# Performance work log

Hardware: AMD Instinct MI355X
Metric: run time of the kernel (lower is better)

The kernel has to match this reference:

```python
import jax, jax.numpy as jnp
import numpy as np

NUM_HEADS = 4  # init kwarg num_heads


def setup_inputs() -> dict:
    key = jax.random.key(0)
    ks = jax.random.split(key, 9)
    B, N, C, S1 = 8, 2048, 128, 3  # S1 = scale + 1
    w = 1.0 / np.sqrt(C)
    return {
        "pcd": jax.random.normal(ks[0], (B, N, C), jnp.float32),
        "coordinate": jax.random.normal(ks[1], (B, N, 3), jnp.float32),
        "K": 16,
        "Wq": jax.random.normal(ks[2], (C, C), jnp.float32) * w,
        "bq": jax.random.normal(ks[3], (C,), jnp.float32) * w,
        "Wk": jax.random.normal(ks[4], (S1, C, C), jnp.float32) * w,
        "bk": jax.random.normal(ks[5], (S1, C), jnp.float32) * w,
        "Wv": jax.random.normal(ks[6], (C, C), jnp.float32) * w,
        "bv": jax.random.normal(ks[7], (C,), jnp.float32) * w,
    }


def reference(pcd, coordinate, K, Wq, bq, Wk, bk, Wv, bv):
    B, N, C = pcd.shape
    S1 = Wk.shape[0]            # scale + 1
    H = NUM_HEADS
    D = C // H                  # head_dim
    Kt = K * S1                 # one KNN shared by all scales ('OneK')

    # --- KNN in coordinate space (squared euclidean) ---
    sq = jnp.sum(coordinate * coordinate, axis=-1)                      # [B,N]
    dist = sq[:, :, None] + sq[:, None, :] \
        - 2.0 * jnp.einsum('bnc,bmc->bnm', coordinate, coordinate)      # [B,N,N]
    _, idx = jax.lax.top_k(-dist, Kt)                                   # [B,N,Kt]

    # --- gather neighbor features, group_type='diff' (neighbor - center) ---
    nb = jax.vmap(lambda f, i: f[i])(pcd, idx)                          # [B,N,Kt,C]
    diff = nb - pcd[:, :, None, :]                                      # [B,N,Kt,C]

    q = (pcd @ Wq + bq).reshape(B, N, H, D)                             # [B,N,H,D]
    v = (pcd @ Wv + bv).reshape(B, N, H, D)                             # [B,N,H,D]
    inv_sqrt_d = 1.0 / jnp.sqrt(jnp.asarray(D, pcd.dtype))

    # --- per-scale attention maps ('multiple' mode), summed to a per-head gate ---
    attn_map = jnp.zeros((B, N, H), pcd.dtype)
    for i in range(S1):
        feats = diff[:, :, i * K:(i + 1) * K, :]                        # [B,N,K,C]
        k_i = (feats @ Wk[i] + bk[i]).reshape(B, N, K, H, D)            # [B,N,K,H,D]
        logits = jnp.einsum('bnhd,bnkhd->bnhk', q, k_i) * inv_sqrt_d    # [B,N,H,K]
        a = jax.nn.softmax(logits, axis=-1)
        attn_map = attn_map + jnp.sum(a * logits, axis=-1)              # [B,N,H]

    # matmul(attn[...,1,1], value[...,1,D]) -> per-head scalar gate on value
    out = attn_map[..., None] * v                                       # [B,N,H,D]
    return out.reshape(B, N, H * D)
```

## Files before the change

### kernel.cpp

```cpp
#include <hip/hip_runtime.h>
#include <hip/hip_bf16.h>
#include <cstdint>
#include <cstddef>

#define NB_B 8
#define NB_N 2048
#define NB_C 128
#define NB_H 4
#define NB_D 32
#define NB_S1 3
#define NB_K 16
#define NB_KT 48
#define INV_SQRT_D 0.17677669529663688f

#define DPP_F(x, ctrl) \
  __int_as_float(__builtin_amdgcn_update_dpp(0, __float_as_int(x), ctrl, 0xF, 0xF, true))

__device__ __forceinline__ float sum16(float x) {
  x += DPP_F(x, 0xB1);
  x += DPP_F(x, 0x4E);
  x += DPP_F(x, 0x141);
  x += DPP_F(x, 0x140);
  return x;
}
__device__ __forceinline__ float max16(float x) {
  x = fmaxf(x, DPP_F(x, 0xB1));
  x = fmaxf(x, DPP_F(x, 0x4E));
  x = fmaxf(x, DPP_F(x, 0x141));
  x = fmaxf(x, DPP_F(x, 0x140));
  return x;
}

__device__ __forceinline__ unsigned long long u64min(unsigned long long a,
                                                     unsigned long long b) {
  return a < b ? a : b;
}
__device__ __forceinline__ unsigned long long u64max(unsigned long long a,
                                                     unsigned long long b) {
  return a > b ? a : b;
}

__device__ __forceinline__ unsigned int dpp32(unsigned int x, int sel) {
  if (sel == 0)
    return (unsigned int)__builtin_amdgcn_update_dpp(0, (int)x, 0xB1, 0xF, 0xF, true);
  return (unsigned int)__builtin_amdgcn_update_dpp(0, (int)x, 0x4E, 0xF, 0xF, true);
}
__device__ __forceinline__ unsigned long long lane_xor64(unsigned long long v, int lx) {
  if (lx == 32) return __shfl_xor(v, 32);
  unsigned int lo = (unsigned int)v, hi = (unsigned int)(v >> 32);
  switch (lx) {
    case 1:  lo = dpp32(lo, 0); hi = dpp32(hi, 0); break;
    case 2:  lo = dpp32(lo, 1); hi = dpp32(hi, 1); break;
    case 4:
      lo = (unsigned int)__builtin_amdgcn_ds_swizzle((int)lo, 0x101F);
      hi = (unsigned int)__builtin_amdgcn_ds_swizzle((int)hi, 0x101F);
      break;
    case 8:
      lo = (unsigned int)__builtin_amdgcn_ds_swizzle((int)lo, 0x201F);
      hi = (unsigned int)__builtin_amdgcn_ds_swizzle((int)hi, 0x201F);
      break;
    default:
      lo = (unsigned int)__builtin_amdgcn_ds_swizzle((int)lo, 0x401F);
      hi = (unsigned int)__builtin_amdgcn_ds_swizzle((int)hi, 0x401F);
      break;
  }
  return ((unsigned long long)hi << 32) | lo;
}

__device__ __forceinline__ void bitonic128(unsigned long long& v0,
                                           unsigned long long& v1, int L) {
#pragma unroll
  for (int k = 2; k <= 128; k <<= 1) {
#pragma unroll
    for (int j = k >> 1; j > 0; j >>= 1) {
      bool up = ((L & (k >> 1)) == 0);
      if (j == 1) {
        unsigned long long lo = u64min(v0, v1), hi = u64max(v0, v1);
        v0 = up ? lo : hi;
        v1 = up ? hi : lo;
      } else {
        int lx = j >> 1;
        unsigned long long o0 = lane_xor64(v0, lx);
        unsigned long long o1 = lane_xor64(v1, lx);
        bool keepmin = (((L & lx) == 0) == up);
        v0 = keepmin ? u64min(v0, o0) : u64max(v0, o0);
        v1 = keepmin ? u64min(v1, o1) : u64max(v1, o1);
      }
    }
  }
}

__global__ __launch_bounds__(256) void prep_kernel(const float* __restrict__ coord,
                                                   const float* __restrict__ Wk,
                                                   float* __restrict__ sq,
                                                   float* __restrict__ wkT) {
  int tid = blockIdx.x * 256 + threadIdx.x;
  if (tid < NB_B * NB_N) {
    float x = coord[tid * 3 + 0], y = coord[tid * 3 + 1], z = coord[tid * 3 + 2];
    sq[tid] = x * x + y * y + z * z;
  }
  if (tid < NB_S1 * NB_C * NB_C) {
    int i = tid >> 14;
    int rem = tid & 16383;
    int col = rem >> 7, c = rem & 127;
    wkT[tid] = Wk[i * 16384 + c * 128 + col];
  }
}

__global__ __launch_bounds__(256) void topk4_kernel(const float* __restrict__ coord,
                                                    const float* __restrict__ sq,
                                                    int* __restrict__ idx_out) {
  __shared__ unsigned long long srv[4][128];
  const int t = threadIdx.x;
  const int w = t >> 6, l = t & 63;
  const int bn = blockIdx.x * 4 + w;
  const int b = bn >> 11, n = bn & 2047;
  const float* cb = coord + (size_t)b * NB_N * 3;
  const float* sqb = sq + b * NB_N;

  const float cx = cb[n * 3 + 0], cy = cb[n * 3 + 1], cz = cb[n * 3 + 2];
  const float sqn = sqb[n];

  unsigned int dk[32];
#pragma unroll
  for (int it = 0; it < 32; ++it) {
    int m = it * 64 + l;
    float mx = cb[m * 3 + 0], my = cb[m * 3 + 1], mz = cb[m * 3 + 2];
    float d = sqn + sqb[m] - 2.f * (cx * mx + cy * my + cz * mz);
    unsigned int db = __float_as_uint(d);
    dk[it] = (db & 0x80000000u) ? ~db : (db | 0x80000000u);
  }

#define KEY(IT) ((((unsigned long long)dk[(IT)]) << 32) | (unsigned int)((IT) * 64 + l))

  unsigned long long m1 = ~0ULL, m2 = ~0ULL;
#pragma unroll
  for (int it = 0; it < 32; ++it) {
    unsigned long long k = KEY(it);
    if (k < m1) { m2 = m1; m1 = k; }
    else if (k < m2) { m2 = k; }
  }

  unsigned long long v0 = m1, v1 = m2;
  bitonic128(v0, v1, l);
  const unsigned long long T = __shfl(v1, 23);

  srv[w][l] = ~0ULL;
  srv[w][l + 64] = ~0ULL;
  int base = 0;
#pragma unroll
  for (int it = 0; it < 32; ++it) {
    unsigned long long k = KEY(it);
    bool pred = (k <= T);
    unsigned long long mask = __ballot(pred);
    int my = base +
             (int)__builtin_amdgcn_mbcnt_hi(
                 (unsigned int)(mask >> 32),
                 __builtin_amdgcn_mbcnt_lo((unsigned int)mask, 0u));
    if (pred && my < 128) srv[w][my] = k;
    base += (int)__popcll(mask);
  }

  if (base <= 128) {
    asm volatile("s_waitcnt lgkmcnt(0)" ::: "memory");
    unsigned long long s0 = srv[w][2 * l];
    unsigned long long s1 = srv[w][2 * l + 1];
    bitonic128(s0, s1, l);
    if (l < 24) {
      int2 o = make_int2((int)(unsigned int)s0, (int)(unsigned int)s1);
      *reinterpret_cast<int2*>(&idx_out[(size_t)bn * NB_KT + 2 * l]) = o;
    }
  } else {
    unsigned int popped = 0;
    unsigned int my_out = 0;
    for (int r = 0; r < NB_KT; ++r) {
      unsigned long long lm = ~0ULL;
      int lslot = 0;
#pragma unroll
      for (int it = 0; it < 32; ++it) {
        unsigned long long k = KEY(it);
        bool ok = ((popped >> it) & 1u) == 0u && k < lm;
        if (ok) { lm = k; lslot = it; }
      }
      unsigned long long g = lm;
#pragma unroll
      for (int lx = 1; lx <= 32; lx <<= 1) {
        unsigned long long o = lane_xor64(g, lx);
        if (o < g) g = o;
      }
      if (l == r) my_out = (unsigned int)g;
      if (lm == g) popped |= (1u << lslot);
    }
    if (l < NB_KT) idx_out[(size_t)bn * NB_KT + l] = (int)my_out;
  }
#undef KEY
}

__global__ __launch_bounds__(256) void main_kernel(
    const float* __restrict__ pcd,
    const float* __restrict__ Wq, const float* __restrict__ bq,
    const float* __restrict__ bk,
    const float* __restrict__ Wv, const float* __restrict__ bv,
    const float* __restrict__ wkT,
    const int* __restrict__ nbr_idx,
    float* __restrict__ out) {
  __shared__ __align__(16) float self_lds[16][128];
  __shared__ __align__(8) float q_lds[16][136];
  __shared__ float qbk_lds[16][12];

  const int t = threadIdx.x;
  const int w = t >> 6, l = t & 63;
  const int h_l = l >> 4, cg = l & 15;
  const int ws = w * 4;
  const int pt_base = blockIdx.x * 16 + ws;
  const float* pcd_b = pcd + (size_t)((blockIdx.x * 16) >> 11) * NB_N * 128;

#pragma unroll
  for (int p = 0; p < 4; ++p) {
    float2 s = reinterpret_cast<const float2*>(pcd + (size_t)(pt_base + p) * 128)[l];
    reinterpret_cast<float2*>(&self_lds[ws + p][0])[l] = s;
  }

  float qa[4] = {0, 0, 0, 0}, qb[4] = {0, 0, 0, 0};
  float va[4] = {0, 0, 0, 0}, vb[4] = {0, 0, 0, 0};
#pragma unroll 4
  for (int c = 0; c < 128; c += 2) {
    float2 wq0 = reinterpret_cast<const float2*>(Wq + c * 128)[l];
    float2 wv0 = reinterpret_cast<const float2*>(Wv + c * 128)[l];
    float2 wq1 = reinterpret_cast<const float2*>(Wq + (c + 1) * 128)[l];
    float2 wv1 = reinterpret_cast<const float2*>(Wv + (c + 1) * 128)[l];
#pragma unroll
    for (int p = 0; p < 4; ++p) {
      float2 x2 = *reinterpret_cast<const float2*>(&self_lds[ws + p][c]);
      qa[p] = fmaf(wq0.x, x2.x, qa[p]); qb[p] = fmaf(wq0.y, x2.x, qb[p]);
      va[p] = fmaf(wv0.x, x2.x, va[p]); vb[p] = fmaf(wv0.y, x2.x, vb[p]);
      qa[p] = fmaf(wq1.x, x2.y, qa[p]); qb[p] = fmaf(wq1.y, x2.y, qb[p]);
      va[p] = fmaf(wv1.x, x2.y, va[p]); vb[p] = fmaf(wv1.y, x2.y, vb[p]);
    }
  }
  {
    float2 bqv = reinterpret_cast<const float2*>(bq)[l];
    float2 bvv = reinterpret_cast<const float2*>(bv)[l];
#pragma unroll
    for (int p = 0; p < 4; ++p) {
      qa[p] += bqv.x; qb[p] += bqv.y; va[p] += bvv.x; vb[p] += bvv.y;
    }
  }
#pragma unroll
  for (int p = 0; p < 4; ++p) {
    *reinterpret_cast<float2*>(&q_lds[ws + p][h_l * 34 + 2 * cg]) =
        make_float2(qa[p], qb[p]);
  }
  if (l < 48) {
    int p = l / 12, g = l % 12;
    int i = g >> 2, h = g & 3;
    const float* qp = &q_lds[ws + p][h * 34];
    const float* bkp = bk + i * 128 + h * 32;
    float s = 0.f;
#pragma unroll 8
    for (int d = 0; d < 32; ++d) s = fmaf(qp[d], bkp[d], s);
    qbk_lds[ws + p][g] = s;
  }

  int nidx[4];
#pragma unroll
  for (int p = 0; p < 4; ++p)
    nidx[p] = (l < 48) ? nbr_idx[(size_t)(pt_base + p) * NB_KT + l] : 0;

  float am[4] = {0, 0, 0, 0};

#pragma unroll
  for (int i = 0; i < 3; ++i) {
    float u[4][8];
#pragma unroll
    for (int p = 0; p < 4; ++p)
#pragma unroll
      for (int k = 0; k < 8; ++k) u[p][k] = 0.f;
    {
      const float* wrow = wkT + i * 16384 + (h_l * 32) * 128 + 4 * cg;
#pragma unroll 4
      for (int d = 0; d < 32; d += 2) {
        float4 wa0 = *reinterpret_cast<const float4*>(wrow + d * 128);
        float4 wb0 = *reinterpret_cast<const float4*>(wrow + d * 128 + 64);
        float4 wa1 = *reinterpret_cast<const float4*>(wrow + (d + 1) * 128);
        float4 wb1 = *reinterpret_cast<const float4*>(wrow + (d + 1) * 128 + 64);
#pragma unroll
        for (int p = 0; p < 4; ++p) {
          float2 qv2 = *reinterpret_cast<const float2*>(&q_lds[ws + p][h_l * 34 + d]);
          u[p][0] = fmaf(wa0.x, qv2.x, u[p][0]);
          u[p][1] = fmaf(wa0.y, qv2.x, u[p][1]);
          u[p][2] = fmaf(wa0.z, qv2.x, u[p][2]);
          u[p][3] = fmaf(wa0.w, qv2.x, u[p][3]);
          u[p][4] = fmaf(wb0.x, qv2.x, u[p][4]);
          u[p][5] = fmaf(wb0.y, qv2.x, u[p][5]);
          u[p][6] = fmaf(wb0.z, qv2.x, u[p][6]);
          u[p][7] = fmaf(wb0.w, qv2.x, u[p][7]);
          u[p][0] = fmaf(wa1.x, qv2.y, u[p][0]);
          u[p][1] = fmaf(wa1.y, qv2.y, u[p][1]);
          u[p][2] = fmaf(wa1.z, qv2.y, u[p][2]);
          u[p][3] = fmaf(wa1.w, qv2.y, u[p][3]);
          u[p][4] = fmaf(wb1.x, qv2.y, u[p][4]);
          u[p][5] = fmaf(wb1.y, qv2.y, u[p][5]);
          u[p][6] = fmaf(wb1.z, qv2.y, u[p][6]);
          u[p][7] = fmaf(wb1.w, qv2.y, u[p][7]);
        }
      }
    }
    float base[4];
#pragma unroll
    for (int p = 0; p < 4; ++p) {
      const float4* sp = reinterpret_cast<const float4*>(&self_lds[ws + p][4 * cg]);
      float4 sA = sp[0];
      float4 sB = sp[16];
      float sd;
      sd = sA.x * u[p][0];
      sd = fmaf(sA.y, u[p][1], sd);
      sd = fmaf(sA.z, u[p][2], sd);
      sd = fmaf(sA.w, u[p][3], sd);
      sd = fmaf(sB.x, u[p][4], sd);
      sd = fmaf(sB.y, u[p][5], sd);
      sd = fmaf(sB.z, u[p][6], sd);
      sd = fmaf(sB.w, u[p][7], sd);
      sd = sum16(sd);
      base[p] = qbk_lds[ws + p][i * 4 + h_l] - sd;
    }
#pragma unroll
    for (int p = 0; p < 4; ++p) {
      float4 sA[4], sB[4];
#define LOADROW(J, SLOT)                                                     \
  {                                                                          \
    int nb_ = __builtin_amdgcn_readlane(nidx[p], i * 16 + (J));              \
    const float* rp_ = pcd_b + (size_t)(unsigned)nb_ * 128 + 4 * cg;         \
    sA[(SLOT)] = *reinterpret_cast<const float4*>(rp_);                      \
    sB[(SLOT)] = *reinterpret_cast<const float4*>(rp_ + 64);                 \
  }
      LOADROW(0, 0) LOADROW(1, 1) LOADROW(2, 2) LOADROW(3, 3)
      float myl = 0.f;
#pragma unroll
      for (int jg = 0; jg < 4; ++jg) {
#pragma unroll
        for (int js = 0; js < 4; ++js) {
          const int j = jg * 4 + js;
          float4 nA = sA[js], nB = sB[js];
          if (jg < 3) LOADROW(j + 4, js)
          float pd;
          pd = nA.x * u[p][0];
          pd = fmaf(nA.y, u[p][1], pd);
          pd = fmaf(nA.z, u[p][2], pd);
          pd = fmaf(nA.w, u[p][3], pd);
          pd = fmaf(nB.x, u[p][4], pd);
          pd = fmaf(nB.y, u[p][5], pd);
          pd = fmaf(nB.z, u[p][6], pd);
          pd = fmaf(nB.w, u[p][7], pd);
          pd = sum16(pd);
          float lg = (pd + base[p]) * INV_SQRT_D;
          if (cg == j) myl = lg;
        }
      }
#undef LOADROW
      float m = max16(myl);
      float e = expf(myl - m);
      float swl = e * myl;
      float se = sum16(e);
      swl = sum16(swl);
      am[p] += swl / se;
    }
  }

#pragma unroll
  for (int p = 0; p < 4; ++p) {
    float2 o = make_float2(am[p] * va[p], am[p] * vb[p]);
    reinterpret_cast<float2*>(out + (size_t)(pt_base + p) * 128)[l] = o;
  }
}

extern "C" void kernel_launch(void* const* d_in, const int* in_sizes, int n_in,
                              void* d_out, int out_size, void* d_ws, size_t ws_size,
                              hipStream_t stream) {
  const float* pcd   = (const float*)d_in[0];
  const float* coord = (const float*)d_in[1];
  const float* Wq = (const float*)d_in[3];
  const float* bq = (const float*)d_in[4];
  const float* Wk = (const float*)d_in[5];
  const float* bk = (const float*)d_in[6];
  const float* Wv = (const float*)d_in[7];
  const float* bv = (const float*)d_in[8];
  float* out = (float*)d_out;

  int*   idx_ws = (int*)d_ws;
  float* sq_ws  = (float*)((char*)d_ws + 3145728);
  float* wkT_ws = (float*)((char*)d_ws + 3211264);

  prep_kernel<<<192, 256, 0, stream>>>(coord, Wk, sq_ws, wkT_ws);
  topk4_kernel<<<NB_B * NB_N / 4, 256, 0, stream>>>(coord, sq_ws, idx_ws);
  main_kernel<<<NB_B * NB_N / 16, 256, 0, stream>>>(pcd, Wq, bq, bk, Wv, bv,
                                                    wkT_ws, idx_ws, out);
}
```

Measured before the change: 246.9 us.

## Recompute distance keys in top-k, add 64-wide sort path, shrink main blocks

The top-k kernel no longer keeps all 32 distance keys in registers. It recomputes them from coordinates on each pass with partial unrolling, which cuts register pressure but repeats the loads and arithmetic. A single-register 64-lane bitonic sort handles the common case where at most 64 candidates pass the threshold, and the 128-wide sort is kept as the fallback. The main kernel moves from 256-thread blocks of 16 points to 128-thread blocks of 8 points, giving twice as many smaller blocks and half the shared memory per block.

```diff
diff --git a/kernel.cpp b/kernel.cpp
--- a/kernel.cpp
+++ b/kernel.cpp
@@ -90,6 +90,20 @@
   }
 }
 
+__device__ __forceinline__ unsigned long long bitonic64(unsigned long long v, int l) {
+#pragma unroll
+  for (int k = 2; k <= 64; k <<= 1) {
+#pragma unroll
+    for (int j = k >> 1; j > 0; j >>= 1) {
+      unsigned long long o = lane_xor64(v, j);
+      bool up = ((l & k) == 0);
+      bool keepmin = (((l & j) == 0) == up);
+      v = keepmin ? u64min(v, o) : u64max(v, o);
+    }
+  }
+  return v;
+}
+
 __global__ __launch_bounds__(256) void prep_kernel(const float* __restrict__ coord,
                                                    const float* __restrict__ Wk,
                                                    float* __restrict__ sq,
@@ -107,7 +121,18 @@
   }
 }
 
-__global__ __launch_bounds__(256) void topk4_kernel(const float* __restrict__ coord,
+__device__ __forceinline__ unsigned int dist_key(const float* __restrict__ cb,
+                                                 const float* __restrict__ sqb,
+                                                 float cx, float cy, float cz,
+                                                 float sqn, int m) {
+  float mx = cb[m * 3 + 0], my = cb[m * 3 + 1], mz = cb[m * 3 + 2];
+  float dot = __fmaf_rn(cz, mz, __fmaf_rn(cy, my, cx * mx));
+  float d = sqn + sqb[m] - 2.f * dot;
+  unsigned int db = __float_as_uint(d);
+  return (db & 0x80000000u) ? ~db : (db | 0x80000000u);
+}
+
+__global__ __launch_bounds__(256) void topk5_kernel(const float* __restrict__ coord,
                                                     const float* __restrict__ sq,
                                                     int* __restrict__ idx_out) {
   __shared__ unsigned long long srv[4][128];
@@ -121,20 +146,13 @@
   const float cx = cb[n * 3 + 0], cy = cb[n * 3 + 1], cz = cb[n * 3 + 2];
   const float sqn = sqb[n];
 
-  unsigned int dk[32];
-#pragma unroll
-  for (int it = 0; it < 32; ++it) {
-    int m = it * 64 + l;
-    float mx = cb[m * 3 + 0], my = cb[m * 3 + 1], mz = cb[m * 3 + 2];
-    float d = sqn + sqb[m] - 2.f * (cx * mx + cy * my + cz * mz);
-    unsigned int db = __float_as_uint(d);
-    dk[it] = (db & 0x80000000u) ? ~db : (db | 0x80000000u);
-  }
-
-#define KEY(IT) ((((unsigned long long)dk[(IT)]) << 32) | (unsigned int)((IT) * 64 + l))
+#define KEY(IT)                                                               \
+  ((((unsigned long long)dist_key(cb, sqb, cx, cy, cz, sqn, (IT) * 64 + l))   \
+    << 32) |                                                                  \
+   (unsigned int)((IT) * 64 + l))
 
   unsigned long long m1 = ~0ULL, m2 = ~0ULL;
-#pragma unroll
+#pragma unroll 8
   for (int it = 0; it < 32; ++it) {
     unsigned long long k = KEY(it);
     if (k < m1) { m2 = m1; m1 = k; }
@@ -147,21 +165,25 @@
 
   srv[w][l] = ~0ULL;
   srv[w][l + 64] = ~0ULL;
-  int base = 0;
-#pragma unroll
+  int M = 0;
+#pragma unroll 8
   for (int it = 0; it < 32; ++it) {
     unsigned long long k = KEY(it);
     bool pred = (k <= T);
     unsigned long long mask = __ballot(pred);
-    int my = base +
+    int my = M +
              (int)__builtin_amdgcn_mbcnt_hi(
                  (unsigned int)(mask >> 32),
                  __builtin_amdgcn_mbcnt_lo((unsigned int)mask, 0u));
     if (pred && my < 128) srv[w][my] = k;
-    base += (int)__popcll(mask);
-  }
-
-  if (base <= 128) {
+    M += (int)__popcll(mask);
+  }
+
+  if (M <= 64) {
+    asm volatile("s_waitcnt lgkmcnt(0)" ::: "memory");
+    unsigned long long s = bitonic64(srv[w][l], l);
+    if (l < NB_KT) idx_out[(size_t)bn * NB_KT + l] = (int)(unsigned int)s;
+  } else if (M <= 128) {
     asm volatile("s_waitcnt lgkmcnt(0)" ::: "memory");
     unsigned long long s0 = srv[w][2 * l];
     unsigned long long s1 = srv[w][2 * l + 1];
@@ -176,7 +198,6 @@
     for (int r = 0; r < NB_KT; ++r) {
       unsigned long long lm = ~0ULL;
       int lslot = 0;
-#pragma unroll
       for (int it = 0; it < 32; ++it) {
         unsigned long long k = KEY(it);
         bool ok = ((popped >> it) & 1u) == 0u && k < lm;
@@ -196,7 +217,7 @@
 #undef KEY
 }
 
-__global__ __launch_bounds__(256) void main_kernel(
+__global__ __launch_bounds__(128) void main_kernel(
     const float* __restrict__ pcd,
     const float* __restrict__ Wq, const float* __restrict__ bq,
     const float* __restrict__ bk,
@@ -204,16 +225,16 @@
     const float* __restrict__ wkT,
     const int* __restrict__ nbr_idx,
     float* __restrict__ out) {
-  __shared__ __align__(16) float self_lds[16][128];
-  __shared__ __align__(8) float q_lds[16][136];
-  __shared__ float qbk_lds[16][12];
+  __shared__ __align__(16) float self_lds[8][128];
+  __shared__ __align__(8) float q_lds[8][136];
+  __shared__ float qbk_lds[8][12];
 
   const int t = threadIdx.x;
   const int w = t >> 6, l = t & 63;
   const int h_l = l >> 4, cg = l & 15;
   const int ws = w * 4;
-  const int pt_base = blockIdx.x * 16 + ws;
-  const float* pcd_b = pcd + (size_t)((blockIdx.x * 16) >> 11) * NB_N * 128;
+  const int pt_base = blockIdx.x * 8 + ws;
+  const float* pcd_b = pcd + (size_t)((blockIdx.x * 8) >> 11) * NB_N * 128;
 
 #pragma unroll
   for (int p = 0; p < 4; ++p) {
@@ -392,7 +413,7 @@
   float* wkT_ws = (float*)((char*)d_ws + 3211264);
 
   prep_kernel<<<192, 256, 0, stream>>>(coord, Wk, sq_ws, wkT_ws);
-  topk4_kernel<<<NB_B * NB_N / 4, 256, 0, stream>>>(coord, sq_ws, idx_ws);
-  main_kernel<<<NB_B * NB_N / 16, 256, 0, stream>>>(pcd, Wq, bq, bk, Wv, bv,
-                                                    wkT_ws, idx_ws, out);
-}
+  topk5_kernel<<<NB_B * NB_N / 4, 256, 0, stream>>>(coord, sq_ws, idx_ws);
+  main_kernel<<<NB_B * NB_N / 8, 128, 0, stream>>>(pcd, Wq, bq, bk, Wv, bv,
+                                                   wkT_ws, idx_ws, out);
+}
```

Measured after the change: 246.3 us. About the same (-0.2%).
